# Kernel optimization log

Hardware: AMD Instinct MI355X
Metric: run time of the kernel (lower is better)

Reference implementation:

```python
import jax, jax.numpy as jnp
import numpy as np

DIM = 1024
N_HEADS = 16
MLP_DIM = 4096
DEPTH = 6
HEAD_DIM = DIM // N_HEADS
SCALE = DIM ** -0.5  # module uses full dim (self.dim_heads = dim), NOT head_dim
EPS = 1e-5


def setup_inputs() -> dict:
    key = jax.random.key(0)
    ks = jax.random.split(key, 12)
    s = lambda k, shape, fan: jax.random.normal(k, shape, jnp.float32) * (fan ** -0.5)
    return {
        "x": jax.random.normal(ks[0], (8, 1024, DIM), jnp.float32),
        "Wq": s(ks[1], (DIM, DIM), DIM), "bq": jnp.zeros((DIM,), jnp.float32),
        "Wk": s(ks[2], (DIM, DIM), DIM), "bk": jnp.zeros((DIM,), jnp.float32),
        "Wv": s(ks[3], (DIM, DIM), DIM), "bv": jnp.zeros((DIM,), jnp.float32),
        "W1": s(ks[4], (DIM, MLP_DIM), DIM), "b1": jnp.zeros((MLP_DIM,), jnp.float32),
        "W2": s(ks[5], (MLP_DIM, DIM), MLP_DIM), "b2": jnp.zeros((DIM,), jnp.float32),
        "gamma": jnp.ones((DIM,), jnp.float32),
        "beta": jnp.zeros((DIM,), jnp.float32),
    }


def _layernorm(x, gamma, beta):
    mu = jnp.mean(x, axis=-1, keepdims=True)
    var = jnp.mean(jnp.square(x - mu), axis=-1, keepdims=True)
    return (x - mu) * jax.lax.rsqrt(var + EPS) * gamma + beta


def _attention(x, Wq, bq, Wk, bk, Wv, bv):
    b, n, _ = x.shape
    split = lambda t: t.reshape(b, n, N_HEADS, HEAD_DIM).transpose(0, 2, 1, 3)  # b h n d
    q = split(x @ Wq + bq)
    k = split(x @ Wk + bk)
    v = split(x @ Wv + bv)
    logit = jnp.einsum('bhnd,bhmd->bhnm', q, k) * SCALE
    attn = jax.nn.softmax(logit, axis=-1)
    out = jnp.einsum('bhnm,bhmd->bhnd', attn, v)
    return out.transpose(0, 2, 1, 3).reshape(b, n, DIM)


def reference(x, Wq, bq, Wk, bk, Wv, bv, W1, b1, W2, b2, gamma, beta):
    # Same single attention + MLP modules (shared weights) applied `depth` times.
    for _ in range(DEPTH):
        x = _attention(_layernorm(x, gamma, beta), Wq, bq, Wk, bk, Wv, bv) + x
        h = _layernorm(x, gamma, beta)
        x = (jax.nn.gelu(h @ W1 + b1, approximate=False) @ W2 + b2) + x
    return x
```

## Files before the change

kernel.cpp:

```cpp
#include <hip/hip_runtime.h>
#include <cstdint>
#include <cmath>

typedef short bf16x8 __attribute__((ext_vector_type(8)));
typedef float f32x4 __attribute__((ext_vector_type(4)));

#define AS_GLOBAL(p) (const __attribute__((address_space(1))) void*)(p)
#define AS_LDS(p)    (__attribute__((address_space(3))) void*)(p)

#define QSCALE 0.04508422002778f

__device__ inline float b2f(unsigned short u) {
    union { unsigned int i; float f; } c; c.i = ((unsigned int)u) << 16; return c.f;
}
__device__ inline unsigned short f2b(float f) {
    return (unsigned short)((__float_as_uint(f) + 0x8000u) >> 16);
}
__device__ inline unsigned cvt_pk_bf16u(float lo, float hi) {
    unsigned r;
    asm("v_cvt_pk_bf16_f32 %0, %1, %2" : "=v"(r) : "v"(lo), "v"(hi));
    return r;
}
__device__ inline float fast_gelu(float x) {
    float arg = -x * (2.30223674f + 0.10294946f * x * x);
    float t = exp2f(arg);
    return x * __builtin_amdgcn_rcpf(1.f + t);
}

__device__ inline bf16x8 ldsfrag(const unsigned short* SM, int base_sh, int r, int lc) {
    return *(const bf16x8*)((const char*)SM + base_sh * 2 + r * 128 + ((lc ^ (r & 7)) << 4));
}

__global__ __launch_bounds__(256) void transpose_f32_to_bf16(
    const float* __restrict__ W, unsigned short* __restrict__ Wt, int K, int N)
{
    __shared__ unsigned short sh[32][33];
    int n0 = blockIdx.x * 32;
    int k0 = blockIdx.y * 32;
    int tr = threadIdx.x >> 5;
    int tc = threadIdx.x & 31;
#pragma unroll
    for (int i = 0; i < 4; i++)
        sh[tr + i * 8][tc] = f2b(W[(size_t)(k0 + tr + i * 8) * N + n0 + tc]);
    __syncthreads();
#pragma unroll
    for (int i = 0; i < 4; i++)
        Wt[(size_t)(n0 + tr + i * 8) * K + k0 + tc] = sh[tc][tr + i * 8];
}

__global__ __launch_bounds__(256) void concat_bias(const float* __restrict__ bq,
                                                   const float* __restrict__ bk,
                                                   float* __restrict__ bqk)
{
    int i = blockIdx.x * 256 + threadIdx.x;
    bqk[i] = (i < 1024) ? bq[i] : bk[i - 1024];
}

__global__ __launch_bounds__(256) void layernorm_k(
    const float* __restrict__ x, const float* __restrict__ gamma,
    const float* __restrict__ beta, unsigned short* __restrict__ out)
{
    int row = blockIdx.x;
    int t = threadIdx.x;
    f32x4 v = *(const f32x4*)(x + (size_t)row * 1024 + t * 4);
    float s  = v[0] + v[1] + v[2] + v[3];
    float s2 = v[0]*v[0] + v[1]*v[1] + v[2]*v[2] + v[3]*v[3];
#pragma unroll
    for (int off = 32; off >= 1; off >>= 1) {
        s  += __shfl_xor(s,  off);
        s2 += __shfl_xor(s2, off);
    }
    __shared__ float red[8];
    int w = t >> 6;
    if ((t & 63) == 0) { red[w] = s; red[4 + w] = s2; }
    __syncthreads();
    s  = red[0] + red[1] + red[2] + red[3];
    s2 = red[4] + red[5] + red[6] + red[7];
    float mu  = s * (1.f / 1024.f);
    float var = s2 * (1.f / 1024.f) - mu * mu;
    float rs  = rsqrtf(var + 1e-5f);
    int c = t * 4;
    f32x4 g = *(const f32x4*)(gamma + c);
    f32x4 be = *(const f32x4*)(beta + c);
    unsigned int lo, hi;
    {
        float o0 = (v[0] - mu) * rs * g[0] + be[0];
        float o1 = (v[1] - mu) * rs * g[1] + be[1];
        float o2 = (v[2] - mu) * rs * g[2] + be[2];
        float o3 = (v[3] - mu) * rs * g[3] + be[3];
        lo = (unsigned)f2b(o0) | ((unsigned)f2b(o1) << 16);
        hi = (unsigned)f2b(o2) | ((unsigned)f2b(o3) << 16);
    }
    uint2 pk; pk.x = lo; pk.y = hi;
    *(uint2*)(out + (size_t)row * 1024 + c) = pk;
}

template<int MODE, int NBNL, int BN, int SMALLM = 0>
__global__ __launch_bounds__(512, 2) void gemm256(
    const unsigned short* __restrict__ A,
    const unsigned short* __restrict__ Bt,
    const float* __restrict__ bias,
    const float* __restrict__ resid,
    void* __restrict__ outp,
    int M, int N, int K)
{
    constexpr int NFR = BN / 64;
    constexpr int WGN = BN / 64;
    constexpr int WM  = 2 * WGN;
    extern __shared__ unsigned short LDS[];

    const int t   = threadIdx.x;
    const int bi  = blockIdx.x;
    const int xcd = bi & 7;
    const int j   = bi >> 3;
    int m_idx, n_idx;
    if (SMALLM) {
        m_idx = j >> 3;
        n_idx = xcd * 8 + (j & 7);
    } else {
        const int mper = M >> 11;
        m_idx = xcd * mper + (j >> NBNL);
        n_idx = j & ((1 << NBNL) - 1);
    }
    const int m0 = m_idx * 256;
    const int n0 = n_idx * BN;

    const int w    = t >> 6;
    const int lane = t & 63;
    const int l15  = lane & 15;
    const int q    = lane >> 4;
    const int wmb  = (w / WGN) * (WM * 16);
    const int wnb  = (w % WGN) * 64;
    const int xsw  = (l15 & 7) << 4;

    const int trow = t >> 3;
    const int csrc = ((t & 7) ^ (trow & 7)) << 3;
    const unsigned short* As0 = A  + (size_t)(m0 + trow) * K + csrc;
    const unsigned short* Bs0 = Bt + (size_t)(n0 + trow) * K + csrc;

    f32x4 acc[WM][4];
#pragma unroll
    for (int i = 0; i < WM; i++)
#pragma unroll
        for (int n = 0; n < 4; n++) acc[i][n] = (f32x4)0.f;

    auto STAGE = [&](int Tn) {
        const int bsel = Tn & 1;
        const size_t kk = (size_t)Tn << 6;
#pragma unroll
        for (int la = 0; la < 4; la++)
            __builtin_amdgcn_global_load_lds(
                AS_GLOBAL(As0 + (size_t)la * 64 * K + kk),
                AS_LDS(LDS + bsel * 16384 + la * 4096 + w * 512), 16, 0, 0);
#pragma unroll
        for (int lb = 0; lb < NFR; lb++)
            __builtin_amdgcn_global_load_lds(
                AS_GLOBAL(Bs0 + (size_t)lb * 64 * K + kk),
                AS_LDS(LDS + 32768 + bsel * (BN * 64) + lb * 4096 + w * 512), 16, 0, 0);
    };

    STAGE(0);
    asm volatile("s_waitcnt vmcnt(0)" ::: "memory");
    __builtin_amdgcn_s_barrier();

    const int NT = K >> 6;
    for (int T = 0; T < NT; T++) {
        if (T + 1 < NT) STAGE(T + 1);
        const char* Ab = (const char*)LDS + (T & 1) * 32768;
        const char* Bb = (const char*)LDS + 65536 + (T & 1) * (BN * 128);
#pragma unroll
        for (int ks = 0; ks < 2; ks++) {
            const int colx = ((ks * 64 + q * 16) ^ xsw);
            bf16x8 bfv[4];
#pragma unroll
            for (int ni = 0; ni < 4; ni++)
                bfv[ni] = *(const bf16x8*)(Bb + (wnb + ni * 16 + l15) * 128 + colx);
#pragma unroll
            for (int mh = 0; mh < 2; mh++) {
                bf16x8 af[WM / 2];
#pragma unroll
                for (int m4 = 0; m4 < WM / 2; m4++)
                    af[m4] = *(const bf16x8*)(Ab + (wmb + (mh * (WM / 2) + m4) * 16 + l15) * 128 + colx);
                __builtin_amdgcn_s_setprio(1);
#pragma unroll
                for (int m4 = 0; m4 < WM / 2; m4++)
#pragma unroll
                    for (int ni = 0; ni < 4; ni++)
                        acc[mh * (WM / 2) + m4][ni] = __builtin_amdgcn_mfma_f32_16x16x32_bf16(
                            af[m4], bfv[ni], acc[mh * (WM / 2) + m4][ni], 0, 0, 0);
                __builtin_amdgcn_s_setprio(0);
                __builtin_amdgcn_sched_barrier(0);
                if (!(ks == 1 && mh == 1)) __builtin_amdgcn_s_barrier();
            }
        }
        asm volatile("s_waitcnt vmcnt(0)" ::: "memory");
        __builtin_amdgcn_s_barrier();
    }

    const float qsc = (MODE == 5 && n0 < 1024) ? QSCALE : 1.f;
#pragma unroll
    for (int mi = 0; mi < WM; mi++) {
        const int gr0 = m0 + wmb + mi * 16 + q * 4;
#pragma unroll
        for (int ni = 0; ni < 4; ni++) {
            const int gc = n0 + wnb + ni * 16 + l15;
            const float bv = (MODE == 3) ? 0.f : bias[gc];
#pragma unroll
            for (int r = 0; r < 4; r++) {
                const int gr = gr0 + r;
                float v = acc[mi][ni][r] + ((MODE == 3) ? bias[gr] : bv);
                if (MODE == 1) {
                    ((unsigned short*)outp)[(size_t)gr * N + gc] = f2b(fast_gelu(v));
                } else if (MODE == 2) {
                    ((float*)outp)[(size_t)gr * N + gc] = resid[(size_t)gr * N + gc] + v;
                } else if (MODE == 3) {
                    ((unsigned short*)outp)[(size_t)gr * N + gc] = f2b(v);
                } else {
                    ((unsigned short*)outp)[(size_t)gr * N + gc] = f2b(v * qsc);
                }
            }
        }
    }
}

__global__ __launch_bounds__(256, 4) void attn_k(
    const unsigned short* __restrict__ qkb,
    const unsigned short* __restrict__ vtb,
    const float* __restrict__ xres,
    float* __restrict__ xout)
{
    __shared__ unsigned short SM[20480];

    const int t    = threadIdx.x;
    const int blk  = blockIdx.x;
    const int qt   = blk >> 7;
    const int bh   = blk & 127;
    const int h    = bh & 15;
    const int b    = bh >> 4;
    const int w    = t >> 6;
    const int lane = t & 63;
    const int l15  = lane & 15;
    const int quad = lane >> 4;
    const int wrow = w * 32;

    const int sr  = t >> 3;
    const int slc = (t & 7) ^ (sr & 7);
    const unsigned short* Qsrc = qkb + ((size_t)(b * 1024 + qt * 128 + sr)) * 2048 + h * 64 + slc * 8;
    const unsigned short* Ksrc = qkb + ((size_t)(b * 1024 + sr)) * 2048 + 1024 + h * 64 + slc * 8;
    const unsigned short* Vsrc = vtb + ((size_t)(h * 64 + sr)) * 8192 + (size_t)b * 1024 + slc * 8;

    auto GLL = [&](const unsigned short* g, int sh) {
        __builtin_amdgcn_global_load_lds(AS_GLOBAL(g), AS_LDS(SM + sh + w * 512), 16, 0, 0);
    };

#pragma unroll
    for (int c = 0; c < 4; c++) GLL(Qsrc + (size_t)c * 32 * 2048, c * 2048);
#pragma unroll
    for (int c = 0; c < 2; c++) GLL(Ksrc + (size_t)c * 32 * 2048, 8192 + c * 2048);
#pragma unroll
    for (int c = 0; c < 2; c++) GLL(Ksrc + (size_t)(64 + c * 32) * 2048, 12288 + c * 2048);
#pragma unroll
    for (int c = 0; c < 2; c++) GLL(Vsrc + (size_t)c * 32 * 8192, 16384 + c * 2048);
    asm volatile("s_waitcnt vmcnt(0)" ::: "memory");
    __builtin_amdgcn_s_barrier();

    bf16x8 qf[2][2];
#pragma unroll
    for (int nt2 = 0; nt2 < 2; nt2++)
#pragma unroll
        for (int kd = 0; kd < 2; kd++)
            qf[nt2][kd] = ldsfrag(SM, 0, wrow + nt2 * 16 + l15, kd * 4 + quad);

    const bf16x8 onesv = (bf16x8)(short)0x3F80;
    float m_s[2] = { -1e30f, -1e30f };
    f32x4 l_acc[2] = { (f32x4)0.f, (f32x4)0.f };
    f32x4 O[2][4];
#pragma unroll
    for (int nt2 = 0; nt2 < 2; nt2++)
#pragma unroll
        for (int dt = 0; dt < 4; dt++) O[nt2][dt] = (f32x4)0.f;

    for (int kt = 0; kt < 16; ++kt) {
        const int cur = kt & 1;
        if (kt > 0) {
            const unsigned short* vs = Vsrc + kt * 64;
            GLL(vs, 16384);
            GLL(vs + (size_t)32 * 8192, 16384 + 2048);
        }

        f32x4 s[4][2];
#pragma unroll
        for (int mt = 0; mt < 4; mt++) {
            bf16x8 kf0 = ldsfrag(SM, 8192 + cur * 4096, mt * 16 + l15, quad);
            bf16x8 kf1 = ldsfrag(SM, 8192 + cur * 4096, mt * 16 + l15, 4 + quad);
#pragma unroll
            for (int nt2 = 0; nt2 < 2; nt2++) {
                f32x4 a = (f32x4)0.f;
                a = __builtin_amdgcn_mfma_f32_16x16x32_bf16(kf0, qf[nt2][0], a, 0, 0, 0);
                a = __builtin_amdgcn_mfma_f32_16x16x32_bf16(kf1, qf[nt2][1], a, 0, 0, 0);
                s[mt][nt2] = a;
            }
        }

#pragma unroll
        for (int nt2 = 0; nt2 < 2; nt2++) {
            float tm = -1e30f;
#pragma unroll
            for (int mt = 0; mt < 4; mt++) {
                f32x4 sv = s[mt][nt2];
                tm = fmaxf(tm, fmaxf(fmaxf(sv[0], sv[1]), fmaxf(sv[2], sv[3])));
            }
            tm = fmaxf(tm, __shfl_xor(tm, 16));
            tm = fmaxf(tm, __shfl_xor(tm, 32));
            if (!__all(tm <= m_s[nt2])) {
                float nm    = fmaxf(m_s[nt2], tm);
                float alpha = exp2f(m_s[nt2] - nm);
                m_s[nt2] = nm;
                l_acc[nt2] *= alpha;
#pragma unroll
                for (int dt = 0; dt < 4; dt++) O[nt2][dt] *= alpha;
            }
            const float nm = m_s[nt2];
            const int r = wrow + nt2 * 16 + l15;
#pragma unroll
            for (int mt = 0; mt < 4; mt++) {
                float p0 = exp2f(s[mt][nt2][0] - nm);
                float p1 = exp2f(s[mt][nt2][1] - nm);
                float p2 = exp2f(s[mt][nt2][2] - nm);
                float p3 = exp2f(s[mt][nt2][3] - nm);
                uint2 pk;
                pk.x = cvt_pk_bf16u(p0, p1);
                pk.y = cvt_pk_bf16u(p2, p3);
                *(uint2*)((char*)SM + r * 128 + (((2 * mt + (quad >> 1)) ^ (r & 7)) << 4)
                          + (quad & 1) * 8) = pk;
            }
        }

        asm volatile("s_waitcnt vmcnt(0)" ::: "memory");
        __builtin_amdgcn_s_barrier();

        if (kt + 2 < 16) {
            const unsigned short* ks = Ksrc + (size_t)(kt + 2) * 64 * 2048;
            GLL(ks, 8192 + cur * 4096);
            GLL(ks + (size_t)32 * 2048, 8192 + cur * 4096 + 2048);
        }

        bf16x8 pf[2][2];
#pragma unroll
        for (int nt2 = 0; nt2 < 2; nt2++)
#pragma unroll
            for (int kc = 0; kc < 2; kc++)
                pf[nt2][kc] = ldsfrag(SM, 0, wrow + nt2 * 16 + l15, kc * 4 + quad);
#pragma unroll
        for (int nt2 = 0; nt2 < 2; nt2++) {
            l_acc[nt2] = __builtin_amdgcn_mfma_f32_16x16x32_bf16(onesv, pf[nt2][0], l_acc[nt2], 0, 0, 0);
            l_acc[nt2] = __builtin_amdgcn_mfma_f32_16x16x32_bf16(onesv, pf[nt2][1], l_acc[nt2], 0, 0, 0);
        }
#pragma unroll
        for (int dt = 0; dt < 4; dt++) {
            bf16x8 vf0 = ldsfrag(SM, 16384, dt * 16 + l15, quad);
            bf16x8 vf1 = ldsfrag(SM, 16384, dt * 16 + l15, 4 + quad);
#pragma unroll
            for (int nt2 = 0; nt2 < 2; nt2++) {
                O[nt2][dt] = __builtin_amdgcn_mfma_f32_16x16x32_bf16(vf0, pf[nt2][0], O[nt2][dt], 0, 0, 0);
                O[nt2][dt] = __builtin_amdgcn_mfma_f32_16x16x32_bf16(vf1, pf[nt2][1], O[nt2][dt], 0, 0, 0);
            }
        }

        __builtin_amdgcn_s_barrier();
    }

    {
        float inv0 = 1.f / l_acc[0][0], inv1 = 1.f / l_acc[1][0];
#pragma unroll
        for (int nt2 = 0; nt2 < 2; nt2++) {
            float inv = (nt2 == 0) ? inv0 : inv1;
            const int r = wrow + nt2 * 16 + l15;
#pragma unroll
            for (int dt = 0; dt < 4; dt++) {
                uint2 pk;
                pk.x = cvt_pk_bf16u(O[nt2][dt][0] * inv, O[nt2][dt][1] * inv);
                pk.y = cvt_pk_bf16u(O[nt2][dt][2] * inv, O[nt2][dt][3] * inv);
                *(uint2*)((char*)SM + 16384 + r * 128 + (((2 * dt + (quad >> 1)) ^ (r & 7)) << 4)
                          + (quad & 1) * 8) = pk;
            }
        }
    }
    __syncthreads();
    {
        int r0 = t >> 2;
        int qc = t & 3;
#pragma unroll
        for (int half = 0; half < 2; half++) {
            int r = r0 + half * 64;
            size_t off = ((size_t)(b * 1024 + qt * 128 + r)) * 1024 + h * 64 + qc * 16;
            const float* xrp = xres + off;
            float* xwp = xout + off;
#pragma unroll
            for (int jj = 0; jj < 2; jj++) {
                uint4 u = *(const uint4*)((const char*)SM + 16384 + r * 128
                                          + (((qc * 2 + jj) ^ (r & 7)) << 4));
                f32x4 xv0 = *(const f32x4*)(xrp + jj * 8);
                f32x4 xv1 = *(const f32x4*)(xrp + jj * 8 + 4);
                xv0[0] += b2f((unsigned short)(u.x & 0xffff));
                xv0[1] += b2f((unsigned short)(u.x >> 16));
                xv0[2] += b2f((unsigned short)(u.y & 0xffff));
                xv0[3] += b2f((unsigned short)(u.y >> 16));
                xv1[0] += b2f((unsigned short)(u.z & 0xffff));
                xv1[1] += b2f((unsigned short)(u.z >> 16));
                xv1[2] += b2f((unsigned short)(u.w & 0xffff));
                xv1[3] += b2f((unsigned short)(u.w >> 16));
                *(f32x4*)(xwp + jj * 8)     = xv0;
                *(f32x4*)(xwp + jj * 8 + 4) = xv1;
            }
        }
    }
}

extern "C" void kernel_launch(void* const* d_in, const int* in_sizes, int n_in,
                              void* d_out, int out_size, void* d_ws, size_t ws_size,
                              hipStream_t stream)
{
    (void)in_sizes; (void)n_in; (void)out_size; (void)ws_size;
    const float* x_in  = (const float*)d_in[0];
    const float* Wq    = (const float*)d_in[1];
    const float* bq    = (const float*)d_in[2];
    const float* Wk    = (const float*)d_in[3];
    const float* bk    = (const float*)d_in[4];
    const float* Wv    = (const float*)d_in[5];
    const float* bv    = (const float*)d_in[6];
    const float* W1    = (const float*)d_in[7];
    const float* b1    = (const float*)d_in[8];
    const float* W2    = (const float*)d_in[9];
    const float* b2    = (const float*)d_in[10];
    const float* gamma = (const float*)d_in[11];
    const float* beta  = (const float*)d_in[12];

    char* base = (char*)d_ws;
    float*          xf   = (float*)(base);
    unsigned short* xn   = (unsigned short*)(base + 33554432);
    unsigned short* qkb  = (unsigned short*)(base + 50331648);
    unsigned short* vtb  = (unsigned short*)(base + 50331648 + 33554432);
    unsigned short* h1   = (unsigned short*)(base + 50331648);
    char* wbase = base + 50331648 + 67108864;
    unsigned short* WqkT = (unsigned short*)(wbase);
    unsigned short* WvT  = (unsigned short*)(wbase + 4194304);
    unsigned short* W1T  = (unsigned short*)(wbase + 6291456);
    unsigned short* W2T  = (unsigned short*)(wbase + 14680064);
    float*          bqk  = (float*)(wbase + 23068672);

    transpose_f32_to_bf16<<<dim3(32, 32),  256, 0, stream>>>(Wq, WqkT, 1024, 1024);
    transpose_f32_to_bf16<<<dim3(32, 32),  256, 0, stream>>>(Wk, WqkT + 1048576, 1024, 1024);
    transpose_f32_to_bf16<<<dim3(32, 32),  256, 0, stream>>>(Wv, WvT, 1024, 1024);
    transpose_f32_to_bf16<<<dim3(128, 32), 256, 0, stream>>>(W1, W1T, 1024, 4096);
    transpose_f32_to_bf16<<<dim3(32, 128), 256, 0, stream>>>(W2, W2T, 4096, 1024);
    concat_bias<<<8, 256, 0, stream>>>(bq, bk, bqk);

    for (int layer = 0; layer < 6; ++layer) {
        const float* xcur = (layer == 0) ? x_in : xf;
        layernorm_k<<<8192, 256, 0, stream>>>(xcur, gamma, beta, xn);
        gemm256<5, 3, 256><<<256, 512, 131072, stream>>>(xn, WqkT, bqk, nullptr, qkb, 8192, 2048, 1024);
        gemm256<3, 0, 128, 1><<<256, 512, 98304, stream>>>(WvT, xn, bv, nullptr, vtb, 1024, 8192, 1024);
        attn_k<<<1024, 256, 0, stream>>>(qkb, vtb, xcur, xf);
        layernorm_k<<<8192, 256, 0, stream>>>(xf, gamma, beta, xn);
        gemm256<1, 4, 256><<<512, 512, 131072, stream>>>(xn, W1T, b1, nullptr, h1, 8192, 4096, 1024);
        float* mout = (layer == 5) ? (float*)d_out : xf;
        gemm256<2, 3, 128><<<256, 512, 98304, stream>>>(h1, W2T, b2, xf, mout, 8192, 1024, 4096);
    }
}
```

Measured before the change: 1.928 ms.

## Software-pipeline LDS fragment reads and split global prefetch across MFMA phases

Restructures the GEMM main loop so the LDS fragment loads for the next MFMA block are issued before the current block runs. Partial lgkmcnt waits replace full waits, and A/B fragments are double-buffered in registers. The global-to-LDS prefetch for the next K tile is split into four parts, one interleaved with each compute phase instead of one burst. This aims to hide LDS and global-load latency behind MFMA work, at the cost of more registers and hand-tuned wait counts that must match the compiler's instruction order.

```diff
diff --git a/kernel.cpp b/kernel.cpp
--- a/kernel.cpp
+++ b/kernel.cpp
@@ -107,6 +107,7 @@
     constexpr int NFR = BN / 64;
     constexpr int WGN = BN / 64;
     constexpr int WM  = 2 * WGN;
+    constexpr int HM  = WM / 2;
     extern __shared__ unsigned short LDS[];
 
     const int t   = threadIdx.x;
@@ -144,57 +145,101 @@
 #pragma unroll
         for (int n = 0; n < 4; n++) acc[i][n] = (f32x4)0.f;
 
-    auto STAGE = [&](int Tn) {
+    auto STAGEP = [&](int Tn, int part) {
         const int bsel = Tn & 1;
         const size_t kk = (size_t)Tn << 6;
-#pragma unroll
-        for (int la = 0; la < 4; la++)
-            __builtin_amdgcn_global_load_lds(
-                AS_GLOBAL(As0 + (size_t)la * 64 * K + kk),
-                AS_LDS(LDS + bsel * 16384 + la * 4096 + w * 512), 16, 0, 0);
-#pragma unroll
-        for (int lb = 0; lb < NFR; lb++)
-            __builtin_amdgcn_global_load_lds(
-                AS_GLOBAL(Bs0 + (size_t)lb * 64 * K + kk),
-                AS_LDS(LDS + 32768 + bsel * (BN * 64) + lb * 4096 + w * 512), 16, 0, 0);
+        if (part < 2) {
+#pragma unroll
+            for (int la = part * 2; la < part * 2 + 2; la++)
+                __builtin_amdgcn_global_load_lds(
+                    AS_GLOBAL(As0 + (size_t)la * 64 * K + kk),
+                    AS_LDS(LDS + bsel * 16384 + la * 4096 + w * 512), 16, 0, 0);
+        } else {
+#pragma unroll
+            for (int lb = (part - 2) * 2; lb < (part - 2) * 2 + 2; lb++)
+                if (lb < NFR)
+                    __builtin_amdgcn_global_load_lds(
+                        AS_GLOBAL(Bs0 + (size_t)lb * 64 * K + kk),
+                        AS_LDS(LDS + 32768 + bsel * (BN * 64) + lb * 4096 + w * 512), 16, 0, 0);
+        }
     };
-
-    STAGE(0);
+    auto RDAF = [&](const char* Ab, int ks, int mh, bf16x8* dst) {
+        const int colx = ((ks * 64 + q * 16) ^ xsw);
+#pragma unroll
+        for (int m4 = 0; m4 < HM; m4++)
+            dst[m4] = *(const bf16x8*)(Ab + (wmb + (mh * HM + m4) * 16 + l15) * 128 + colx);
+    };
+    auto RDBV = [&](const char* Bb, int ks, bf16x8* dst) {
+        const int colx = ((ks * 64 + q * 16) ^ xsw);
+#pragma unroll
+        for (int ni = 0; ni < 4; ni++)
+            dst[ni] = *(const bf16x8*)(Bb + (wnb + ni * 16 + l15) * 128 + colx);
+    };
+    auto MM = [&](int mh, bf16x8* afs, bf16x8* bvs) {
+        __builtin_amdgcn_s_setprio(1);
+#pragma unroll
+        for (int m4 = 0; m4 < HM; m4++)
+#pragma unroll
+            for (int ni = 0; ni < 4; ni++)
+                acc[mh * HM + m4][ni] = __builtin_amdgcn_mfma_f32_16x16x32_bf16(
+                    afs[m4], bvs[ni], acc[mh * HM + m4][ni], 0, 0, 0);
+        __builtin_amdgcn_s_setprio(0);
+        __builtin_amdgcn_sched_barrier(0);
+    };
+
+    bf16x8 afA[HM], afB[HM], bvA[4], bvB[4];
+
+    STAGEP(0, 0); STAGEP(0, 1); STAGEP(0, 2); STAGEP(0, 3);
     asm volatile("s_waitcnt vmcnt(0)" ::: "memory");
     __builtin_amdgcn_s_barrier();
+    RDBV((const char*)LDS + 65536, 0, bvA);
+    RDAF((const char*)LDS, 0, 0, afA);
 
     const int NT = K >> 6;
     for (int T = 0; T < NT; T++) {
-        if (T + 1 < NT) STAGE(T + 1);
         const char* Ab = (const char*)LDS + (T & 1) * 32768;
         const char* Bb = (const char*)LDS + 65536 + (T & 1) * (BN * 128);
-#pragma unroll
-        for (int ks = 0; ks < 2; ks++) {
-            const int colx = ((ks * 64 + q * 16) ^ xsw);
-            bf16x8 bfv[4];
-#pragma unroll
-            for (int ni = 0; ni < 4; ni++)
-                bfv[ni] = *(const bf16x8*)(Bb + (wnb + ni * 16 + l15) * 128 + colx);
-#pragma unroll
-            for (int mh = 0; mh < 2; mh++) {
-                bf16x8 af[WM / 2];
-#pragma unroll
-                for (int m4 = 0; m4 < WM / 2; m4++)
-                    af[m4] = *(const bf16x8*)(Ab + (wmb + (mh * (WM / 2) + m4) * 16 + l15) * 128 + colx);
-                __builtin_amdgcn_s_setprio(1);
-#pragma unroll
-                for (int m4 = 0; m4 < WM / 2; m4++)
-#pragma unroll
-                    for (int ni = 0; ni < 4; ni++)
-                        acc[mh * (WM / 2) + m4][ni] = __builtin_amdgcn_mfma_f32_16x16x32_bf16(
-                            af[m4], bfv[ni], acc[mh * (WM / 2) + m4][ni], 0, 0, 0);
-                __builtin_amdgcn_s_setprio(0);
-                __builtin_amdgcn_sched_barrier(0);
-                if (!(ks == 1 && mh == 1)) __builtin_amdgcn_s_barrier();
-            }
-        }
+        const bool pf = (T + 1 < NT);
+
+        RDAF(Ab, 0, 1, afB);
+        if (pf) STAGEP(T + 1, 0);
+        __builtin_amdgcn_s_barrier();
+        if (BN == 256) asm volatile("s_waitcnt lgkmcnt(4)" ::: "memory");
+        else           asm volatile("s_waitcnt lgkmcnt(2)" ::: "memory");
+        __builtin_amdgcn_sched_barrier(0);
+        MM(0, afA, bvA);
+
+        RDBV(Bb, 1, bvB);
+        RDAF(Ab, 1, 0, afA);
+        if (pf) STAGEP(T + 1, 1);
+        __builtin_amdgcn_s_barrier();
+        if (BN == 256) asm volatile("s_waitcnt lgkmcnt(8)" ::: "memory");
+        else           asm volatile("s_waitcnt lgkmcnt(6)" ::: "memory");
+        __builtin_amdgcn_sched_barrier(0);
+        MM(1, afB, bvA);
+
+        RDAF(Ab, 1, 1, afB);
+        if (pf) STAGEP(T + 1, 2);
+        __builtin_amdgcn_s_barrier();
+        if (BN == 256) asm volatile("s_waitcnt lgkmcnt(4)" ::: "memory");
+        else           asm volatile("s_waitcnt lgkmcnt(2)" ::: "memory");
+        __builtin_amdgcn_sched_barrier(0);
+        MM(0, afA, bvB);
+
+        if (pf) STAGEP(T + 1, 3);
+        __builtin_amdgcn_s_barrier();
+        asm volatile("s_waitcnt lgkmcnt(0)" ::: "memory");
+        __builtin_amdgcn_sched_barrier(0);
+        MM(1, afB, bvB);
+
         asm volatile("s_waitcnt vmcnt(0)" ::: "memory");
         __builtin_amdgcn_s_barrier();
+        if (pf) {
+            const char* AbN = (const char*)LDS + ((T + 1) & 1) * 32768;
+            const char* BbN = (const char*)LDS + 65536 + ((T + 1) & 1) * (BN * 128);
+            RDBV(BbN, 0, bvA);
+            RDAF(AbN, 0, 0, afA);
+        }
     }
 
     const float qsc = (MODE == 5 && n0 < 1024) ? QSCALE : 1.f;
```

After: 1.877 ms. -2.7%, faster.
